# Optimization experiments

Hardware: AMD Instinct MI355X
Metric: run time of the kernel (lower is better)

Reference implementation:

```python
import jax, jax.numpy as jnp
import numpy as np

B, N, C = 8, 1024, 768
NUM_HEADS = 12
HEAD_DIM = C // NUM_HEADS  # 64
WS = 32                    # window_size[0] == window_size[1] == H == W
REL_DIM = 2 * WS - 1       # 63


def setup_inputs() -> dict:
    key = jax.random.key(0)
    ks = jax.random.split(key, 7)
    x = jax.random.normal(ks[0], (B, N, C), dtype=jnp.float32)
    qkv_w = jax.random.normal(ks[1], (3 * C, C), dtype=jnp.float32) * 0.02
    qkv_b = jnp.zeros((3 * C,), dtype=jnp.float32)
    proj_w = jax.random.normal(ks[2], (C, C), dtype=jnp.float32) * 0.02
    proj_b = jnp.zeros((C,), dtype=jnp.float32)
    rel_pos_h = jax.random.normal(ks[3], (REL_DIM, HEAD_DIM), dtype=jnp.float32) * 0.02
    rel_pos_w = jax.random.normal(ks[4], (REL_DIM, HEAD_DIM), dtype=jnp.float32) * 0.02
    return {
        "x": x,
        "qkv_w": qkv_w,
        "qkv_b": qkv_b,
        "proj_w": proj_w,
        "proj_b": proj_b,
        "rel_pos_h": rel_pos_h,
        "rel_pos_w": rel_pos_w,
        "H": WS,
        "W": WS,
    }


def reference(x, qkv_w, qkv_b, proj_w, proj_b, rel_pos_h, rel_pos_w, H, W):
    B_, N_, C_ = x.shape
    heads = NUM_HEADS
    hd = C_ // heads
    scale = hd ** -0.5

    # qkv projection: (B, N, 3, heads, hd) -> (3, B, heads, N, hd)
    qkv = (x @ qkv_w.T + qkv_b).reshape(B_, N_, 3, heads, hd).transpose(2, 0, 3, 1, 4)
    q, k, v = qkv[0], qkv[1], qkv[2]
    q = q * scale

    # raw scores (B, heads, N, N)
    attn = jnp.einsum('bhqd,bhkd->bhqk', q, k)

    # decomposed relative position bias (q_shape == k_shape -> ratios are 1.0)
    dist_h = jnp.arange(H)[:, None] - jnp.arange(H)[None, :] + (H - 1)
    dist_w = jnp.arange(W)[:, None] - jnp.arange(W)[None, :] + (W - 1)
    Rh = rel_pos_h[dist_h]  # (H, H, hd)
    Rw = rel_pos_w[dist_w]  # (W, W, hd)

    r_q = q.reshape(B_, heads, H, W, hd)
    rel_h = jnp.einsum('byhwc,hkc->byhwk', r_q, Rh)  # (B, heads, H, W, k_h)
    rel_w = jnp.einsum('byhwc,wkc->byhwk', r_q, Rw)  # (B, heads, H, W, k_w)

    attn = (attn.reshape(B_, heads, H, W, H, W)
            + rel_h[:, :, :, :, :, None]
            + rel_w[:, :, :, :, None, :]).reshape(B_, heads, N_, N_)

    attn = jax.nn.softmax(attn, axis=-1)
    out = jnp.einsum('bhqk,bhkd->bhqd', attn, v)
    out = out.transpose(0, 2, 1, 3).reshape(B_, N_, heads * hd)
    return out @ proj_w.T + proj_b
```

## Files before the change

### kernel.cpp

```cpp
#include <hip/hip_runtime.h>
#include <cstddef>

typedef short s8v __attribute__((ext_vector_type(8)));
typedef float f4v __attribute__((ext_vector_type(4)));

__device__ __forceinline__ unsigned short f2bf(float f) {
    union { float f; unsigned u; } v; v.f = f;
    unsigned r = v.u + 0x7fff + ((v.u >> 16) & 1);
    return (unsigned short)(r >> 16);
}
__device__ __forceinline__ float bf2f(unsigned short u) {
    union { unsigned u; float f; } v; v.u = ((unsigned)u) << 16;
    return v.f;
}

__device__ __forceinline__ void gl_lds16(const void* g, void* l) {
    __builtin_amdgcn_global_load_lds(
        (const __attribute__((address_space(1))) void*)g,
        (__attribute__((address_space(3))) void*)l, 16, 0, 0);
}

__global__ __launch_bounds__(256) void to_bf16(
    const float* __restrict__ s, unsigned short* __restrict__ d, int n8)
{
    int i = blockIdx.x * 256 + threadIdx.x;
    if (i < n8) {
        float4 f0 = ((const float4*)s)[i * 2];
        float4 f1 = ((const float4*)s)[i * 2 + 1];
        uint4 pk;
        pk.x = (unsigned)f2bf(f0.x) | ((unsigned)f2bf(f0.y) << 16);
        pk.y = (unsigned)f2bf(f0.z) | ((unsigned)f2bf(f0.w) << 16);
        pk.z = (unsigned)f2bf(f1.x) | ((unsigned)f2bf(f1.y) << 16);
        pk.w = (unsigned)f2bf(f1.z) | ((unsigned)f2bf(f1.w) << 16);
        ((uint4*)d)[i] = pk;
    }
}

__global__ __launch_bounds__(256) void qkv_gemm_mfma(
    const unsigned short* __restrict__ A, const unsigned short* __restrict__ W,
    const float* __restrict__ bias,
    float* __restrict__ qb, unsigned short* __restrict__ kb,
    unsigned short* __restrict__ vb)
{
    __shared__ __align__(16) unsigned short As[128 * 32];
    __shared__ __align__(16) unsigned short Bs[128 * 32];
    const int t     = threadIdx.x;
    const int bc    = blockIdx.x;
    const int br    = blockIdx.y;
    const int wv    = t >> 6;
    const int lane  = t & 63;
    const int col16 = lane & 15;
    const int quad  = lane >> 4;
    const int w4    = lane >> 2;
    const int k8    = (lane & 3) << 3;
    const int mw    = wv >> 1, nw = wv & 1;

    const unsigned short* Ag = A + (size_t)(br * 128 + (wv << 5) + w4) * 768 + k8;
    const unsigned short* Wg = W + (size_t)(bc * 128 + (wv << 5) + w4) * 768 + k8;
    unsigned short* Asw = &As[(wv << 5) * 32];
    unsigned short* Bsw = &Bs[(wv << 5) * 32];

    f4v acc[4][4];
#pragma unroll
    for (int mt = 0; mt < 4; ++mt)
#pragma unroll
        for (int nt = 0; nt < 4; ++nt) {
            acc[mt][nt][0] = 0.f; acc[mt][nt][1] = 0.f;
            acc[mt][nt][2] = 0.f; acc[mt][nt][3] = 0.f;
        }

    for (int k0 = 0; k0 < 768; k0 += 32) {
        __syncthreads();
        gl_lds16(Ag + k0,             Asw);
        gl_lds16(Ag + k0 + 16 * 768,  Asw + 16 * 32);
        gl_lds16(Wg + k0,             Bsw);
        gl_lds16(Wg + k0 + 16 * 768,  Bsw + 16 * 32);
        __syncthreads();

        s8v a[4], b[4];
#pragma unroll
        for (int mt = 0; mt < 4; ++mt)
            a[mt] = *(const s8v*)&As[(mw * 64 + mt * 16 + col16) * 32 + quad * 8];
#pragma unroll
        for (int nt = 0; nt < 4; ++nt)
            b[nt] = *(const s8v*)&Bs[(nw * 64 + nt * 16 + col16) * 32 + quad * 8];
#pragma unroll
        for (int mt = 0; mt < 4; ++mt)
#pragma unroll
            for (int nt = 0; nt < 4; ++nt)
                acc[mt][nt] = __builtin_amdgcn_mfma_f32_16x16x32_bf16(
                    a[mt], b[nt], acc[mt][nt], 0, 0, 0);
    }

    const int which = bc / 6;
    const int cb    = (bc % 6) * 128 + nw * 64;
    const int m0    = br * 128 + mw * 64 + quad * 4;
#pragma unroll
    for (int nt = 0; nt < 4; ++nt) {
        int c    = cb + nt * 16 + col16;
        int head = c >> 6, d = c & 63;
        float bv = bias[which * 768 + c];
#pragma unroll
        for (int mt = 0; mt < 4; ++mt) {
#pragma unroll
            for (int i = 0; i < 4; ++i) {
                int m   = m0 + mt * 16 + i;
                int bbk = m >> 10, tok = m & 1023;
                size_t idx = (((size_t)(bbk * 12 + head) << 10) + tok) * 64 + d;
                float val = acc[mt][nt][i] + bv;
                if (which == 0)      qb[idx] = val * 0.125f;
                else if (which == 1) kb[idx] = f2bf(val);
                else                 vb[idx] = f2bf(val);
            }
        }
    }
}

__global__ __launch_bounds__(256) void proj_gemm_mfma(
    const unsigned short* __restrict__ A, const unsigned short* __restrict__ W,
    const float* __restrict__ bias, float* __restrict__ Out)
{
    __shared__ __align__(16) unsigned short As[128 * 32];
    __shared__ __align__(16) unsigned short Bs[128 * 32];
    const int t     = threadIdx.x;
    const int bc    = blockIdx.x;
    const int br    = blockIdx.y;
    const int wv    = t >> 6;
    const int lane  = t & 63;
    const int col16 = lane & 15;
    const int quad  = lane >> 4;
    const int w4    = lane >> 2;
    const int k8    = (lane & 3) << 3;
    const int mw    = wv >> 1, nw = wv & 1;

    const unsigned short* Ag = A + (size_t)(br * 128 + (wv << 5) + w4) * 768 + k8;
    const unsigned short* Wg = W + (size_t)(bc * 128 + (wv << 5) + w4) * 768 + k8;
    unsigned short* Asw = &As[(wv << 5) * 32];
    unsigned short* Bsw = &Bs[(wv << 5) * 32];

    f4v acc[4][4];
#pragma unroll
    for (int mt = 0; mt < 4; ++mt)
#pragma unroll
        for (int nt = 0; nt < 4; ++nt) {
            acc[mt][nt][0] = 0.f; acc[mt][nt][1] = 0.f;
            acc[mt][nt][2] = 0.f; acc[mt][nt][3] = 0.f;
        }

    for (int k0 = 0; k0 < 768; k0 += 32) {
        __syncthreads();
        gl_lds16(Ag + k0,             Asw);
        gl_lds16(Ag + k0 + 16 * 768,  Asw + 16 * 32);
        gl_lds16(Wg + k0,             Bsw);
        gl_lds16(Wg + k0 + 16 * 768,  Bsw + 16 * 32);
        __syncthreads();

        s8v a[4], b[4];
#pragma unroll
        for (int mt = 0; mt < 4; ++mt)
            a[mt] = *(const s8v*)&As[(mw * 64 + mt * 16 + col16) * 32 + quad * 8];
#pragma unroll
        for (int nt = 0; nt < 4; ++nt)
            b[nt] = *(const s8v*)&Bs[(nw * 64 + nt * 16 + col16) * 32 + quad * 8];
#pragma unroll
        for (int mt = 0; mt < 4; ++mt)
#pragma unroll
            for (int nt = 0; nt < 4; ++nt)
                acc[mt][nt] = __builtin_amdgcn_mfma_f32_16x16x32_bf16(
                    a[mt], b[nt], acc[mt][nt], 0, 0, 0);
    }

    const int m0 = br * 128 + mw * 64 + quad * 4;
#pragma unroll
    for (int nt = 0; nt < 4; ++nt) {
        int c    = bc * 128 + nw * 64 + nt * 16 + col16;
        float bv = bias[c];
#pragma unroll
        for (int mt = 0; mt < 4; ++mt) {
#pragma unroll
            for (int i = 0; i < 4; ++i) {
                int m = m0 + mt * 16 + i;
                Out[(size_t)m * 768 + c] = acc[mt][nt][i] + bv;
            }
        }
    }
}

__global__ __launch_bounds__(256) void v_transpose(
    const unsigned short* __restrict__ V, unsigned short* __restrict__ Vt)
{
    __shared__ unsigned short Ls[64][72];
    const int t  = threadIdx.x;
    const int tc = blockIdx.x;
    const int bh = blockIdx.y;
    const unsigned short* src = V + (size_t)bh * 65536 + tc * 64 * 64;

    {
        int tok = t >> 2, dg = (t & 3) << 4;
        *(uint4*)&Ls[tok][dg]     = *(const uint4*)(src + tok * 64 + dg);
        *(uint4*)&Ls[tok][dg + 8] = *(const uint4*)(src + tok * 64 + dg + 8);
    }
    __syncthreads();
    {
        int d = t & 63, tg = (t >> 6) << 4;
        unsigned short tmp[16];
#pragma unroll
        for (int i = 0; i < 16; ++i) tmp[i] = Ls[tg + i][d];
        unsigned short* dst = Vt + (size_t)bh * 65536 + (size_t)d * 1024 + tc * 64 + tg;
        *(uint4*)&dst[0] = *(uint4*)&tmp[0];
        *(uint4*)&dst[8] = *(uint4*)&tmp[8];
    }
}

__global__ __launch_bounds__(256) void bias_prep_mfma(
    const float* __restrict__ Q, const float* __restrict__ Rh,
    const float* __restrict__ Rw, unsigned short* __restrict__ qhb,
    unsigned short* __restrict__ qwb)
{
    __shared__ __align__(16) char smem[36864];
    unsigned short (*Qs)[72]  = (unsigned short (*)[72])smem;
    unsigned short (*Rs)[72]  = (unsigned short (*)[72])(smem + 18432);
    unsigned short (*Wsm)[72] = (unsigned short (*)[72])(smem + 27648);
    float (*G)[66]            = (float (*)[66])smem;

    const int t    = threadIdx.x;
    const int tc8  = blockIdx.x;
    const int bh   = blockIdx.y;
    const int tok0 = tc8 << 7;

    for (int id = t; id < 1024; id += 256) {
        int row = id >> 3, g8 = (id & 7) << 3;
        const float* src = Q + ((size_t)bh * 1024 + tok0 + row) * 64 + g8;
        float4 a = *(const float4*)src;
        float4 b = *(const float4*)(src + 4);
        unsigned short* dst = &Qs[row][g8];
        dst[0] = f2bf(a.x); dst[1] = f2bf(a.y); dst[2] = f2bf(a.z); dst[3] = f2bf(a.w);
        dst[4] = f2bf(b.x); dst[5] = f2bf(b.y); dst[6] = f2bf(b.z); dst[7] = f2bf(b.w);
    }
    for (int id = t; id < 512; id += 256) {
        int row = id >> 3, g8 = (id & 7) << 3;
        unsigned short* dh = &Rs[row][g8];
        unsigned short* dw = &Wsm[row][g8];
        if (row < 63) {
            const float* sh = Rh + row * 64 + g8;
            const float* sw = Rw + row * 64 + g8;
            float4 a = *(const float4*)sh; float4 b = *(const float4*)(sh + 4);
            float4 c = *(const float4*)sw; float4 d = *(const float4*)(sw + 4);
            dh[0] = f2bf(a.x); dh[1] = f2bf(a.y); dh[2] = f2bf(a.z); dh[3] = f2bf(a.w);
            dh[4] = f2bf(b.x); dh[5] = f2bf(b.y); dh[6] = f2bf(b.z); dh[7] = f2bf(b.w);
            dw[0] = f2bf(c.x); dw[1] = f2bf(c.y); dw[2] = f2bf(c.z); dw[3] = f2bf(c.w);
            dw[4] = f2bf(d.x); dw[5] = f2bf(d.y); dw[6] = f2bf(d.z); dw[7] = f2bf(d.w);
        } else {
#pragma unroll
            for (int j = 0; j < 8; ++j) { dh[j] = 0; dw[j] = 0; }
        }
    }
    __syncthreads();

    const int wv    = t >> 6;
    const int lane  = t & 63;
    const int col16 = lane & 15;
    const int quad  = lane >> 4;
    const int r0    = wv << 5;

    s8v qa[2][2], rb[4][2], wb[4][2];
#pragma unroll
    for (int mt = 0; mt < 2; ++mt)
#pragma unroll
        for (int kc = 0; kc < 2; ++kc)
            qa[mt][kc] = *(const s8v*)&Qs[r0 + mt * 16 + col16][kc * 32 + quad * 8];
#pragma unroll
    for (int nt = 0; nt < 4; ++nt)
#pragma unroll
        for (int kc = 0; kc < 2; ++kc) {
            rb[nt][kc] = *(const s8v*)&Rs[nt * 16 + col16][kc * 32 + quad * 8];
            wb[nt][kc] = *(const s8v*)&Wsm[nt * 16 + col16][kc * 32 + quad * 8];
        }

    f4v ah[2][4], aw[2][4];
#pragma unroll
    for (int mt = 0; mt < 2; ++mt)
#pragma unroll
        for (int nt = 0; nt < 4; ++nt) {
            f4v z; z[0] = 0.f; z[1] = 0.f; z[2] = 0.f; z[3] = 0.f;
            ah[mt][nt] = z; aw[mt][nt] = z;
        }
#pragma unroll
    for (int mt = 0; mt < 2; ++mt)
#pragma unroll
        for (int nt = 0; nt < 4; ++nt) {
            ah[mt][nt] = __builtin_amdgcn_mfma_f32_16x16x32_bf16(qa[mt][0], rb[nt][0], ah[mt][nt], 0, 0, 0);
            ah[mt][nt] = __builtin_amdgcn_mfma_f32_16x16x32_bf16(qa[mt][1], rb[nt][1], ah[mt][nt], 0, 0, 0);
            aw[mt][nt] = __builtin_amdgcn_mfma_f32_16x16x32_bf16(qa[mt][0], wb[nt][0], aw[mt][nt], 0, 0, 0);
            aw[mt][nt] = __builtin_amdgcn_mfma_f32_16x16x32_bf16(qa[mt][1], wb[nt][1], aw[mt][nt], 0, 0, 0);
        }
    __syncthreads();

#pragma unroll
    for (int mt = 0; mt < 2; ++mt)
#pragma unroll
        for (int nt = 0; nt < 4; ++nt)
#pragma unroll
            for (int i = 0; i < 4; ++i)
                G[r0 + mt * 16 + quad * 4 + i][nt * 16 + col16] = ah[mt][nt][i];
    __syncthreads();
    for (int id = t; id < 2048; id += 256) {
        int tok = id >> 4, c2 = (id & 15) << 1;
        int i_img = (tc8 << 2) + (tok >> 5);
        float g0 = G[tok][i_img - c2 + 31];
        float g1 = G[tok][i_img - c2 + 30];
        unsigned pk = (unsigned)f2bf(g0) | ((unsigned)f2bf(g1) << 16);
        *(unsigned*)&qhb[(((size_t)bh << 10) + tok0 + tok) * 32 + c2] = pk;
    }
    __syncthreads();

#pragma unroll
    for (int mt = 0; mt < 2; ++mt)
#pragma unroll
        for (int nt = 0; nt < 4; ++nt)
#pragma unroll
            for (int i = 0; i < 4; ++i)
                G[r0 + mt * 16 + quad * 4 + i][nt * 16 + col16] = aw[mt][nt][i];
    __syncthreads();
    for (int id = t; id < 2048; id += 256) {
        int tok = id >> 4, c2 = (id & 15) << 1;
        int j = tok & 31;
        float g0 = G[tok][j - c2 + 31];
        float g1 = G[tok][j - c2 + 30];
        unsigned pk = (unsigned)f2bf(g0) | ((unsigned)f2bf(g1) << 16);
        *(unsigned*)&qwb[(((size_t)bh << 10) + tok0 + tok) * 32 + c2] = pk;
    }
}

__global__ __launch_bounds__(256, 4) void attn_mfma(
    const float* __restrict__ Q, const unsigned short* __restrict__ K,
    const unsigned short* __restrict__ Vt,
    const unsigned short* __restrict__ qhb, const unsigned short* __restrict__ qwb,
    unsigned short* __restrict__ Out)
{
    const int t  = threadIdx.x;
    const int id  = blockIdx.x;
    const int xcd = id & 7;
    const int wq  = id >> 3;
    const int bh  = xcd * 12 + (wq % 12);
    const int qt2 = wq / 12;
    const int b   = bh / 12;
    const int h   = bh - b * 12;
    const int q0  = qt2 << 6;

    __shared__ __align__(16) unsigned short Ks[64 * 72];
    __shared__ __align__(16) unsigned short Vs[64 * 72];
    __shared__ __align__(16) unsigned short Pl[64 * 72];
    __shared__ float qh_s[64][32];

    const unsigned short* Kp = K  + (size_t)bh * 65536;
    const unsigned short* Vp = Vt + (size_t)bh * 65536;

    {
        const unsigned* qhp = (const unsigned*)(qhb + ((size_t)bh * 1024 + q0) * 32);
        for (int i2 = t; i2 < 1024; i2 += 256) {
            int row = i2 >> 4, c2 = (i2 & 15) << 1;
            unsigned ph = qhp[i2];
            qh_s[row][c2]     = bf2f((unsigned short)(ph & 0xffff));
            qh_s[row][c2 + 1] = bf2f((unsigned short)(ph >> 16));
        }
    }

    const int wv    = t >> 6;
    const int lane  = t & 63;
    const int col16 = lane & 15;
    const int quad  = lane >> 4;
    const int qrow0 = wv << 4;

    s8v qa0, qa1;
    {
        const float* qsrc = Q + ((size_t)bh * 1024 + q0 + qrow0 + col16) * 64 + quad * 8;
        float4 v0 = *(const float4*)qsrc;
        float4 v1 = *(const float4*)(qsrc + 4);
        float4 v2 = *(const float4*)(qsrc + 32);
        float4 v3 = *(const float4*)(qsrc + 36);
        s8v f0, f1;
        f0[0] = (short)f2bf(v0.x); f0[1] = (short)f2bf(v0.y);
        f0[2] = (short)f2bf(v0.z); f0[3] = (short)f2bf(v0.w);
        f0[4] = (short)f2bf(v1.x); f0[5] = (short)f2bf(v1.y);
        f0[6] = (short)f2bf(v1.z); f0[7] = (short)f2bf(v1.w);
        f1[0] = (short)f2bf(v2.x); f1[1] = (short)f2bf(v2.y);
        f1[2] = (short)f2bf(v2.z); f1[3] = (short)f2bf(v2.w);
        f1[4] = (short)f2bf(v3.x); f1[5] = (short)f2bf(v3.y);
        f1[6] = (short)f2bf(v3.z); f1[7] = (short)f2bf(v3.w);
        qa0 = f0; qa1 = f1;
    }

    float qwr[4][2];
#pragma unroll
    for (int i = 0; i < 4; ++i) {
        size_t row = (size_t)bh * 1024 + q0 + qrow0 + quad * 4 + i;
        qwr[i][0] = bf2f(qwb[row * 32 + col16]);
        qwr[i][1] = bf2f(qwb[row * 32 + col16 + 16]);
    }

    {
        uint4 pk0, pk1, pv0, pv1;
        int e0 = t * 8, e1 = t * 8 + 2048;
        pk0 = *(const uint4*)(Kp + e0);
        pk1 = *(const uint4*)(Kp + e1);
        pv0 = *(const uint4*)(Vp + (size_t)(e0 >> 6) * 1024 + (e0 & 63));
        pv1 = *(const uint4*)(Vp + (size_t)(e1 >> 6) * 1024 + (e1 & 63));
        *(uint4*)&Ks[(e0 >> 6) * 72 + (e0 & 63)] = pk0;
        *(uint4*)&Ks[(e1 >> 6) * 72 + (e1 & 63)] = pk1;
        *(uint4*)&Vs[(e0 >> 6) * 72 + (e0 & 63)] = pv0;
        *(uint4*)&Vs[(e1 >> 6) * 72 + (e1 & 63)] = pv1;
    }
    __syncthreads();

    f4v o[4];
#pragma unroll
    for (int nt = 0; nt < 4; ++nt) { o[nt][0] = 0.f; o[nt][1] = 0.f; o[nt][2] = 0.f; o[nt][3] = 0.f; }
    float lp[4] = {0.f, 0.f, 0.f, 0.f};

    const int e0 = t * 8, e1 = t * 8 + 2048;
    for (int kt = 0; kt < 16; ++kt) {
        uint4 pk0, pk1, pv0, pv1;
        if (kt < 15) {
            const int k0n = (kt + 1) << 6;
            pk0 = *(const uint4*)(Kp + (size_t)k0n * 64 + e0);
            pk1 = *(const uint4*)(Kp + (size_t)k0n * 64 + e1);
            pv0 = *(const uint4*)(Vp + (size_t)(e0 >> 6) * 1024 + k0n + (e0 & 63));
            pv1 = *(const uint4*)(Vp + (size_t)(e1 >> 6) * 1024 + k0n + (e1 & 63));
        }

        f4v s4[4];
#pragma unroll
        for (int nt = 0; nt < 4; ++nt) {
            s8v b0 = *(const s8v*)&Ks[(nt * 16 + col16) * 72 + quad * 8];
            s8v b1 = *(const s8v*)&Ks[(nt * 16 + col16) * 72 + 32 + quad * 8];
            f4v acc; acc[0] = 0.f; acc[1] = 0.f; acc[2] = 0.f; acc[3] = 0.f;
            acc = __builtin_amdgcn_mfma_f32_16x16x32_bf16(qa0, b0, acc, 0, 0, 0);
            acc = __builtin_amdgcn_mfma_f32_16x16x32_bf16(qa1, b1, acc, 0, 0, 0);
            s4[nt] = acc;
        }

        float qh0[4], qh1[4];
#pragma unroll
        for (int i = 0; i < 4; ++i) {
            qh0[i] = qh_s[qrow0 + quad * 4 + i][(kt << 1) + 0];
            qh1[i] = qh_s[qrow0 + quad * 4 + i][(kt << 1) + 1];
        }

#pragma unroll
        for (int nt = 0; nt < 4; ++nt) {
#pragma unroll
            for (int i = 0; i < 4; ++i) {
                float s  = s4[nt][i] + ((nt < 2) ? qh0[i] : qh1[i]) + qwr[i][nt & 1];
                float pe = __expf(s - 16.0f);
                lp[i] += pe;
                Pl[(qrow0 + quad * 4 + i) * 72 + nt * 16 + col16] = f2bf(pe);
            }
        }
        asm volatile("s_waitcnt lgkmcnt(0)" ::: "memory");

        s8v pa0 = *(const s8v*)&Pl[(qrow0 + col16) * 72 + quad * 8];
        s8v pa1 = *(const s8v*)&Pl[(qrow0 + col16) * 72 + 32 + quad * 8];
#pragma unroll
        for (int nt = 0; nt < 4; ++nt) {
            s8v vb0 = *(const s8v*)&Vs[(nt * 16 + col16) * 72 + quad * 8];
            s8v vb1 = *(const s8v*)&Vs[(nt * 16 + col16) * 72 + 32 + quad * 8];
            o[nt] = __builtin_amdgcn_mfma_f32_16x16x32_bf16(pa0, vb0, o[nt], 0, 0, 0);
            o[nt] = __builtin_amdgcn_mfma_f32_16x16x32_bf16(pa1, vb1, o[nt], 0, 0, 0);
        }

        __syncthreads();
        if (kt < 15) {
            *(uint4*)&Ks[(e0 >> 6) * 72 + (e0 & 63)] = pk0;
            *(uint4*)&Ks[(e1 >> 6) * 72 + (e1 & 63)] = pk1;
            *(uint4*)&Vs[(e0 >> 6) * 72 + (e0 & 63)] = pv0;
            *(uint4*)&Vs[(e1 >> 6) * 72 + (e1 & 63)] = pv1;
        }
        __syncthreads();
    }

#pragma unroll
    for (int i = 0; i < 4; ++i) {
#pragma unroll
        for (int m = 8; m >= 1; m >>= 1) lp[i] += __shfl_xor(lp[i], m, 16);
    }
#pragma unroll
    for (int i = 0; i < 4; ++i) {
        float inv = 1.f / lp[i];
        int   qr  = q0 + qrow0 + quad * 4 + i;
        unsigned short* dst = Out + ((size_t)b * 1024 + qr) * 768 + h * 64;
#pragma unroll
        for (int nt = 0; nt < 4; ++nt)
            dst[nt * 16 + col16] = f2bf(o[nt][i] * inv);
    }
}

extern "C" void kernel_launch(void* const* d_in, const int* in_sizes, int n_in,
                              void* d_out, int out_size, void* d_ws, size_t ws_size,
                              hipStream_t stream) {
    const float* x      = (const float*)d_in[0];
    const float* qkv_w  = (const float*)d_in[1];
    const float* qkv_b  = (const float*)d_in[2];
    const float* proj_w = (const float*)d_in[3];
    const float* proj_b = (const float*)d_in[4];
    const float* rel_h  = (const float*)d_in[5];
    const float* rel_w  = (const float*)d_in[6];
    float* out = (float*)d_out;

    char* ws = (char*)d_ws;
    float*          qbuf  = (float*)(ws);
    unsigned short* kbuf  = (unsigned short*)(ws + 25165824);
    unsigned short* vbuf  = (unsigned short*)(ws + 37748736);
    unsigned short* vtbuf = (unsigned short*)(ws + 50331648);
    unsigned short* xab   = (unsigned short*)(ws + 62914560);
    unsigned short* wqb   = (unsigned short*)(ws + 75497472);
    unsigned short* wpb   = (unsigned short*)(ws + 79036416);
    unsigned short* qhb   = vbuf;
    unsigned short* qwb   = vbuf + 3145728;

    to_bf16<<<3072, 256, 0, stream>>>(x,      xab, 786432);
    to_bf16<<<864,  256, 0, stream>>>(qkv_w,  wqb, 221184);
    to_bf16<<<288,  256, 0, stream>>>(proj_w, wpb, 73728);

    qkv_gemm_mfma<<<dim3(18, 64), 256, 0, stream>>>(xab, wqb, qkv_b, qbuf, kbuf, vbuf);
    v_transpose<<<dim3(16, 96), 256, 0, stream>>>(vbuf, vtbuf);
    bias_prep_mfma<<<dim3(8, 96), 256, 0, stream>>>(qbuf, rel_h, rel_w, qhb, qwb);
    attn_mfma<<<1536, 256, 0, stream>>>(qbuf, kbuf, vtbuf, qhb, qwb, xab);
    proj_gemm_mfma<<<dim3(6, 64), 256, 0, stream>>>(xab, wpb, proj_b, out);
}
```

Baseline: 249.0 us.

## Fuse bf16 conversions, store Q as bf16, write V transposed from QKV GEMM

Merges the three fp32-to-bf16 conversion launches into one kernel. The QKV GEMM epilogue now stores Q as bf16 (pre-scaled) and writes V directly in transposed layout, which removes the separate v_transpose kernel and the fp32 Q buffer traffic. The bias-prep and attention kernels read bf16 Q without converting it. LDS padding for the P tile and the qh table is changed to alter bank mapping. The transposed V stores are 8-byte scattered writes, which may coalesce poorly.

```diff
diff --git a/kernel.cpp b/kernel.cpp
--- a/kernel.cpp
+++ b/kernel.cpp
@@ -1,6 +1,7 @@
 #include <hip/hip_runtime.h>
 #include <cstddef>
 
+typedef short s4v __attribute__((ext_vector_type(4)));
 typedef short s8v __attribute__((ext_vector_type(8)));
 typedef float f4v __attribute__((ext_vector_type(4)));
 
@@ -20,27 +21,31 @@
         (__attribute__((address_space(3))) void*)l, 16, 0, 0);
 }
 
-__global__ __launch_bounds__(256) void to_bf16(
-    const float* __restrict__ s, unsigned short* __restrict__ d, int n8)
+__global__ __launch_bounds__(256) void to_bf16_all(
+    const float* __restrict__ x, const float* __restrict__ qw,
+    const float* __restrict__ pw, unsigned short* __restrict__ xd,
+    unsigned short* __restrict__ qd, unsigned short* __restrict__ pd)
 {
     int i = blockIdx.x * 256 + threadIdx.x;
-    if (i < n8) {
-        float4 f0 = ((const float4*)s)[i * 2];
-        float4 f1 = ((const float4*)s)[i * 2 + 1];
-        uint4 pk;
-        pk.x = (unsigned)f2bf(f0.x) | ((unsigned)f2bf(f0.y) << 16);
-        pk.y = (unsigned)f2bf(f0.z) | ((unsigned)f2bf(f0.w) << 16);
-        pk.z = (unsigned)f2bf(f1.x) | ((unsigned)f2bf(f1.y) << 16);
-        pk.w = (unsigned)f2bf(f1.z) | ((unsigned)f2bf(f1.w) << 16);
-        ((uint4*)d)[i] = pk;
-    }
+    const float* s; unsigned short* d; int j;
+    if (i < 786432)       { s = x;  d = xd; j = i; }
+    else if (i < 1007616) { s = qw; d = qd; j = i - 786432; }
+    else                  { s = pw; d = pd; j = i - 1007616; }
+    float4 f0 = ((const float4*)s)[j * 2];
+    float4 f1 = ((const float4*)s)[j * 2 + 1];
+    uint4 pk;
+    pk.x = (unsigned)f2bf(f0.x) | ((unsigned)f2bf(f0.y) << 16);
+    pk.y = (unsigned)f2bf(f0.z) | ((unsigned)f2bf(f0.w) << 16);
+    pk.z = (unsigned)f2bf(f1.x) | ((unsigned)f2bf(f1.y) << 16);
+    pk.w = (unsigned)f2bf(f1.z) | ((unsigned)f2bf(f1.w) << 16);
+    ((uint4*)d)[j] = pk;
 }
 
 __global__ __launch_bounds__(256) void qkv_gemm_mfma(
     const unsigned short* __restrict__ A, const unsigned short* __restrict__ W,
     const float* __restrict__ bias,
-    float* __restrict__ qb, unsigned short* __restrict__ kb,
-    unsigned short* __restrict__ vb)
+    unsigned short* __restrict__ qb, unsigned short* __restrict__ kb,
+    unsigned short* __restrict__ vt)
 {
     __shared__ __align__(16) unsigned short As[128 * 32];
     __shared__ __align__(16) unsigned short Bs[128 * 32];
@@ -95,22 +100,41 @@
     const int which = bc / 6;
     const int cb    = (bc % 6) * 128 + nw * 64;
     const int m0    = br * 128 + mw * 64 + quad * 4;
-#pragma unroll
-    for (int nt = 0; nt < 4; ++nt) {
-        int c    = cb + nt * 16 + col16;
-        int head = c >> 6, d = c & 63;
-        float bv = bias[which * 768 + c];
-#pragma unroll
-        for (int mt = 0; mt < 4; ++mt) {
-#pragma unroll
-            for (int i = 0; i < 4; ++i) {
-                int m   = m0 + mt * 16 + i;
-                int bbk = m >> 10, tok = m & 1023;
-                size_t idx = (((size_t)(bbk * 12 + head) << 10) + tok) * 64 + d;
-                float val = acc[mt][nt][i] + bv;
-                if (which == 0)      qb[idx] = val * 0.125f;
-                else if (which == 1) kb[idx] = f2bf(val);
-                else                 vb[idx] = f2bf(val);
+    if (which == 2) {
+#pragma unroll
+        for (int nt = 0; nt < 4; ++nt) {
+            int c    = cb + nt * 16 + col16;
+            int head = c >> 6, d = c & 63;
+            float bv = bias[1536 + c];
+#pragma unroll
+            for (int mt = 0; mt < 4; ++mt) {
+                int mb  = m0 + mt * 16;
+                int bbk = mb >> 10, tok = mb & 1023;
+                uint2 pk;
+                pk.x = (unsigned)f2bf(acc[mt][nt][0] + bv)
+                     | ((unsigned)f2bf(acc[mt][nt][1] + bv) << 16);
+                pk.y = (unsigned)f2bf(acc[mt][nt][2] + bv)
+                     | ((unsigned)f2bf(acc[mt][nt][3] + bv) << 16);
+                *(uint2*)&vt[((size_t)(bbk * 12 + head)) * 65536 + (size_t)d * 1024 + tok] = pk;
+            }
+        }
+    } else {
+        const float sc = (which == 0) ? 0.125f : 1.0f;
+        unsigned short* dst = (which == 0) ? qb : kb;
+#pragma unroll
+        for (int nt = 0; nt < 4; ++nt) {
+            int c    = cb + nt * 16 + col16;
+            int head = c >> 6, d = c & 63;
+            float bv = bias[which * 768 + c];
+#pragma unroll
+            for (int mt = 0; mt < 4; ++mt) {
+#pragma unroll
+                for (int i = 0; i < 4; ++i) {
+                    int m   = m0 + mt * 16 + i;
+                    int bbk = m >> 10, tok = m & 1023;
+                    dst[(((size_t)(bbk * 12 + head) << 10) + tok) * 64 + d] =
+                        f2bf((acc[mt][nt][i] + bv) * sc);
+                }
             }
         }
     }
@@ -186,34 +210,8 @@
     }
 }
 
-__global__ __launch_bounds__(256) void v_transpose(
-    const unsigned short* __restrict__ V, unsigned short* __restrict__ Vt)
-{
-    __shared__ unsigned short Ls[64][72];
-    const int t  = threadIdx.x;
-    const int tc = blockIdx.x;
-    const int bh = blockIdx.y;
-    const unsigned short* src = V + (size_t)bh * 65536 + tc * 64 * 64;
-
-    {
-        int tok = t >> 2, dg = (t & 3) << 4;
-        *(uint4*)&Ls[tok][dg]     = *(const uint4*)(src + tok * 64 + dg);
-        *(uint4*)&Ls[tok][dg + 8] = *(const uint4*)(src + tok * 64 + dg + 8);
-    }
-    __syncthreads();
-    {
-        int d = t & 63, tg = (t >> 6) << 4;
-        unsigned short tmp[16];
-#pragma unroll
-        for (int i = 0; i < 16; ++i) tmp[i] = Ls[tg + i][d];
-        unsigned short* dst = Vt + (size_t)bh * 65536 + (size_t)d * 1024 + tc * 64 + tg;
-        *(uint4*)&dst[0] = *(uint4*)&tmp[0];
-        *(uint4*)&dst[8] = *(uint4*)&tmp[8];
-    }
-}
-
 __global__ __launch_bounds__(256) void bias_prep_mfma(
-    const float* __restrict__ Q, const float* __restrict__ Rh,
+    const unsigned short* __restrict__ Q, const float* __restrict__ Rh,
     const float* __restrict__ Rw, unsigned short* __restrict__ qhb,
     unsigned short* __restrict__ qwb)
 {
@@ -230,12 +228,8 @@
 
     for (int id = t; id < 1024; id += 256) {
         int row = id >> 3, g8 = (id & 7) << 3;
-        const float* src = Q + ((size_t)bh * 1024 + tok0 + row) * 64 + g8;
-        float4 a = *(const float4*)src;
-        float4 b = *(const float4*)(src + 4);
-        unsigned short* dst = &Qs[row][g8];
-        dst[0] = f2bf(a.x); dst[1] = f2bf(a.y); dst[2] = f2bf(a.z); dst[3] = f2bf(a.w);
-        dst[4] = f2bf(b.x); dst[5] = f2bf(b.y); dst[6] = f2bf(b.z); dst[7] = f2bf(b.w);
+        *(uint4*)&Qs[row][g8] =
+            *(const uint4*)(Q + ((size_t)bh * 1024 + tok0 + row) * 64 + g8);
     }
     for (int id = t; id < 512; id += 256) {
         int row = id >> 3, g8 = (id & 7) << 3;
@@ -333,7 +327,7 @@
 }
 
 __global__ __launch_bounds__(256, 4) void attn_mfma(
-    const float* __restrict__ Q, const unsigned short* __restrict__ K,
+    const unsigned short* __restrict__ Q, const unsigned short* __restrict__ K,
     const unsigned short* __restrict__ Vt,
     const unsigned short* __restrict__ qhb, const unsigned short* __restrict__ qwb,
     unsigned short* __restrict__ Out)
@@ -350,8 +344,8 @@
 
     __shared__ __align__(16) unsigned short Ks[64 * 72];
     __shared__ __align__(16) unsigned short Vs[64 * 72];
-    __shared__ __align__(16) unsigned short Pl[64 * 72];
-    __shared__ float qh_s[64][32];
+    __shared__ __align__(16) unsigned short Pl[64 * 68];
+    __shared__ float qh_s[64][33];
 
     const unsigned short* Kp = K  + (size_t)bh * 65536;
     const unsigned short* Vp = Vt + (size_t)bh * 65536;
@@ -374,21 +368,10 @@
 
     s8v qa0, qa1;
     {
-        const float* qsrc = Q + ((size_t)bh * 1024 + q0 + qrow0 + col16) * 64 + quad * 8;
-        float4 v0 = *(const float4*)qsrc;
-        float4 v1 = *(const float4*)(qsrc + 4);
-        float4 v2 = *(const float4*)(qsrc + 32);
-        float4 v3 = *(const float4*)(qsrc + 36);
-        s8v f0, f1;
-        f0[0] = (short)f2bf(v0.x); f0[1] = (short)f2bf(v0.y);
-        f0[2] = (short)f2bf(v0.z); f0[3] = (short)f2bf(v0.w);
-        f0[4] = (short)f2bf(v1.x); f0[5] = (short)f2bf(v1.y);
-        f0[6] = (short)f2bf(v1.z); f0[7] = (short)f2bf(v1.w);
-        f1[0] = (short)f2bf(v2.x); f1[1] = (short)f2bf(v2.y);
-        f1[2] = (short)f2bf(v2.z); f1[3] = (short)f2bf(v2.w);
-        f1[4] = (short)f2bf(v3.x); f1[5] = (short)f2bf(v3.y);
-        f1[6] = (short)f2bf(v3.z); f1[7] = (short)f2bf(v3.w);
-        qa0 = f0; qa1 = f1;
+        const unsigned short* qsrc =
+            Q + ((size_t)bh * 1024 + q0 + qrow0 + col16) * 64 + quad * 8;
+        qa0 = *(const s8v*)qsrc;
+        qa1 = *(const s8v*)(qsrc + 32);
     }
 
     float qwr[4][2];
@@ -429,7 +412,7 @@
             pv1 = *(const uint4*)(Vp + (size_t)(e1 >> 6) * 1024 + k0n + (e1 & 63));
         }
 
-        f4v s4[4];
+        f4v s4a[4];
 #pragma unroll
         for (int nt = 0; nt < 4; ++nt) {
             s8v b0 = *(const s8v*)&Ks[(nt * 16 + col16) * 72 + quad * 8];
@@ -437,7 +420,7 @@
             f4v acc; acc[0] = 0.f; acc[1] = 0.f; acc[2] = 0.f; acc[3] = 0.f;
             acc = __builtin_amdgcn_mfma_f32_16x16x32_bf16(qa0, b0, acc, 0, 0, 0);
             acc = __builtin_amdgcn_mfma_f32_16x16x32_bf16(qa1, b1, acc, 0, 0, 0);
-            s4[nt] = acc;
+            s4a[nt] = acc;
         }
 
         float qh0[4], qh1[4];
@@ -451,16 +434,21 @@
         for (int nt = 0; nt < 4; ++nt) {
 #pragma unroll
             for (int i = 0; i < 4; ++i) {
-                float s  = s4[nt][i] + ((nt < 2) ? qh0[i] : qh1[i]) + qwr[i][nt & 1];
+                float s  = s4a[nt][i] + ((nt < 2) ? qh0[i] : qh1[i]) + qwr[i][nt & 1];
                 float pe = __expf(s - 16.0f);
                 lp[i] += pe;
-                Pl[(qrow0 + quad * 4 + i) * 72 + nt * 16 + col16] = f2bf(pe);
+                Pl[(qrow0 + quad * 4 + i) * 68 + nt * 16 + col16] = f2bf(pe);
             }
         }
         asm volatile("s_waitcnt lgkmcnt(0)" ::: "memory");
 
-        s8v pa0 = *(const s8v*)&Pl[(qrow0 + col16) * 72 + quad * 8];
-        s8v pa1 = *(const s8v*)&Pl[(qrow0 + col16) * 72 + 32 + quad * 8];
+        const unsigned short* prow = &Pl[(qrow0 + col16) * 68];
+        s4v p0l = *(const s4v*)(prow + quad * 8);
+        s4v p0h = *(const s4v*)(prow + quad * 8 + 4);
+        s4v p1l = *(const s4v*)(prow + 32 + quad * 8);
+        s4v p1h = *(const s4v*)(prow + 36 + quad * 8);
+        s8v pa0 = __builtin_shufflevector(p0l, p0h, 0, 1, 2, 3, 4, 5, 6, 7);
+        s8v pa1 = __builtin_shufflevector(p1l, p1h, 0, 1, 2, 3, 4, 5, 6, 7);
 #pragma unroll
         for (int nt = 0; nt < 4; ++nt) {
             s8v vb0 = *(const s8v*)&Vs[(nt * 16 + col16) * 72 + quad * 8];
@@ -508,22 +496,17 @@
     float* out = (float*)d_out;
 
     char* ws = (char*)d_ws;
-    float*          qbuf  = (float*)(ws);
-    unsigned short* kbuf  = (unsigned short*)(ws + 25165824);
-    unsigned short* vbuf  = (unsigned short*)(ws + 37748736);
-    unsigned short* vtbuf = (unsigned short*)(ws + 50331648);
-    unsigned short* xab   = (unsigned short*)(ws + 62914560);
-    unsigned short* wqb   = (unsigned short*)(ws + 75497472);
-    unsigned short* wpb   = (unsigned short*)(ws + 79036416);
-    unsigned short* qhb   = vbuf;
-    unsigned short* qwb   = vbuf + 3145728;
-
-    to_bf16<<<3072, 256, 0, stream>>>(x,      xab, 786432);
-    to_bf16<<<864,  256, 0, stream>>>(qkv_w,  wqb, 221184);
-    to_bf16<<<288,  256, 0, stream>>>(proj_w, wpb, 73728);
-
-    qkv_gemm_mfma<<<dim3(18, 64), 256, 0, stream>>>(xab, wqb, qkv_b, qbuf, kbuf, vbuf);
-    v_transpose<<<dim3(16, 96), 256, 0, stream>>>(vbuf, vtbuf);
+    unsigned short* qbuf  = (unsigned short*)(ws);
+    unsigned short* kbuf  = (unsigned short*)(ws + 12582912);
+    unsigned short* vtbuf = (unsigned short*)(ws + 25165824);
+    unsigned short* xab   = (unsigned short*)(ws + 37748736);
+    unsigned short* wqb   = (unsigned short*)(ws + 50331648);
+    unsigned short* wpb   = (unsigned short*)(ws + 53870592);
+    unsigned short* qhb   = (unsigned short*)(ws + 55050240);
+    unsigned short* qwb   = (unsigned short*)(ws + 61341696);
+
+    to_bf16_all<<<4224, 256, 0, stream>>>(x, qkv_w, proj_w, xab, wqb, wpb);
+    qkv_gemm_mfma<<<dim3(18, 64), 256, 0, stream>>>(xab, wqb, qkv_b, qbuf, kbuf, vtbuf);
     bias_prep_mfma<<<dim3(8, 96), 256, 0, stream>>>(qbuf, rel_h, rel_w, qhb, qwb);
     attn_mfma<<<1536, 256, 0, stream>>>(qbuf, kbuf, vtbuf, qhb, qwb, xab);
     proj_gemm_mfma<<<dim3(6, 64), 256, 0, stream>>>(xab, wpb, proj_b, out);
```

Result: faster. 240.1 us (-3.6%).
